# Kernel tuning notes

Measured on AMD Instinct MI355X. Metric: run time of the kernel, lower is better.

Reference implementation:

```python
import jax, jax.numpy as jnp
import numpy as np

D_MODEL = 512
NHEAD = 8
D_K = D_MODEL // NHEAD


def setup_inputs() -> dict:
    key = jax.random.key(0)
    ks = jax.random.split(key, 9)
    s = 1.0 / np.sqrt(D_MODEL)
    x = jax.random.normal(ks[0], (2, 2048, D_MODEL), dtype=jnp.float32)
    # torch Linear weights: [out_features, in_features]
    Wq = jax.random.uniform(ks[1], (D_MODEL, D_MODEL), jnp.float32, -s, s)
    bq = jax.random.uniform(ks[2], (D_MODEL,), jnp.float32, -s, s)
    Wk = jax.random.uniform(ks[3], (D_MODEL, D_MODEL), jnp.float32, -s, s)
    bk = jax.random.uniform(ks[4], (D_MODEL,), jnp.float32, -s, s)
    Wv = jax.random.uniform(ks[5], (D_MODEL, D_MODEL), jnp.float32, -s, s)
    bv = jax.random.uniform(ks[6], (D_MODEL,), jnp.float32, -s, s)
    Wo = jax.random.uniform(ks[7], (D_MODEL, D_MODEL), jnp.float32, -s, s)
    bo = jax.random.uniform(ks[8], (D_MODEL,), jnp.float32, -s, s)
    return {"x": x, "Wq": Wq, "bq": bq, "Wk": Wk, "bk": bk,
            "Wv": Wv, "bv": bv, "Wo": Wo, "bo": bo}


def reference(x, Wq, bq, Wk, bk, Wv, bv, Wo, bo):
    B, S, D = x.shape
    H, Dk = NHEAD, D_K

    def proj(W, b):
        # torch Linear: x @ W.T + b -> [B, S, D] -> [B, H, S, Dk]
        y = jnp.einsum('bsd,ed->bse', x, W) + b
        return y.reshape(B, S, H, Dk).transpose(0, 2, 1, 3)

    q = proj(Wq, bq)
    k = proj(Wk, bk)
    v = proj(Wv, bv)

    scores = jnp.einsum('bhqd,bhkd->bhqk', q, k) / jnp.sqrt(jnp.float32(Dk))
    attn = jax.nn.softmax(scores, axis=-1)  # explicit O(S^2) attention matrix
    out = jnp.einsum('bhqk,bhkd->bhqd', attn, v)
    out = out.transpose(0, 2, 1, 3).reshape(B, S, D)
    return jnp.einsum('bsd,ed->bse', out, Wo) + bo
```

## Files before the change

### kernel.cpp

```cpp
#include <hip/hip_runtime.h>

typedef __bf16 bf16_t;
typedef bf16_t bf16x8 __attribute__((ext_vector_type(8)));
typedef bf16_t bf16x4 __attribute__((ext_vector_type(4)));
typedef float  floatx4 __attribute__((ext_vector_type(4)));

#define D_MODEL 512
#define NHEAD   8
#define DK      64
#define BATCH   2
#define SEQ     2048
#define MTOT    (BATCH*SEQ)
#define QSCALE  0.18033688011112042591f

static __device__ __forceinline__ floatx4 mfma16(bf16x8 a, bf16x8 b, floatx4 c) {
    return __builtin_amdgcn_mfma_f32_16x16x32_bf16(a, b, c, 0, 0, 0);
}

__global__ __launch_bounds__(256)
void qkv_proj(const float* __restrict__ x,
              const float* __restrict__ Wq, const float* __restrict__ bq,
              const float* __restrict__ Wk, const float* __restrict__ bk,
              const float* __restrict__ Wv, const float* __restrict__ bv,
              bf16_t* __restrict__ q_ws, bf16_t* __restrict__ k_ws,
              bf16_t* __restrict__ vt_ws)
{
    __shared__ bf16_t Asq[128 * 40];
    __shared__ bf16_t Bsq[128 * 40];

    const int mtile = blockIdx.x;
    const int ntile = blockIdx.y;
    const int which = ntile >> 2;
    const int nsub  = ntile & 3;
    const float* W    = (which == 0) ? Wq : (which == 1) ? Wk : Wv;
    const float* bias = (which == 0) ? bq : (which == 1) ? bk : bv;

    const int tid  = threadIdx.x;
    const int lane = tid & 63;
    const int wave = tid >> 6;
    const int wm = wave & 1, wn = wave >> 1;
    const int l15 = lane & 15, quad = lane >> 4;

    const int m0 = mtile * 128;
    const int n0 = nsub * 128;
    const int srow = tid >> 3;
    const int sseg = tid & 7;

    floatx4 acc[4][4] = {};

    for (int k0 = 0; k0 < 512; k0 += 32) {
        __syncthreads();
        #pragma unroll
        for (int rep = 0; rep < 4; ++rep) {
            const int r = srow + rep * 32;
            const float4 va = *(const float4*)(x + (size_t)(m0 + r) * 512 + k0 + sseg * 4);
            bf16x4 pa; pa[0]=(bf16_t)va.x; pa[1]=(bf16_t)va.y; pa[2]=(bf16_t)va.z; pa[3]=(bf16_t)va.w;
            *(bf16x4*)(&Asq[r * 40 + sseg * 4]) = pa;
            const float4 vb = *(const float4*)(W + (size_t)(n0 + r) * 512 + k0 + sseg * 4);
            bf16x4 pb; pb[0]=(bf16_t)vb.x; pb[1]=(bf16_t)vb.y; pb[2]=(bf16_t)vb.z; pb[3]=(bf16_t)vb.w;
            *(bf16x4*)(&Bsq[r * 40 + sseg * 4]) = pb;
        }
        __syncthreads();

        bf16x8 af[4], bfr[4];
        #pragma unroll
        for (int i = 0; i < 4; ++i)
            af[i] = *(const bf16x8*)(&Asq[(wm * 64 + i * 16 + l15) * 40 + quad * 8]);
        #pragma unroll
        for (int j = 0; j < 4; ++j)
            bfr[j] = *(const bf16x8*)(&Bsq[(wn * 64 + j * 16 + l15) * 40 + quad * 8]);
        #pragma unroll
        for (int i = 0; i < 4; ++i)
            #pragma unroll
            for (int j = 0; j < 4; ++j)
                acc[i][j] = mfma16(af[i], bfr[j], acc[i][j]);
    }

    const float scale = (which == 0) ? QSCALE : 1.0f;
    #pragma unroll
    for (int j = 0; j < 4; ++j) {
        const int e = n0 + wn * 64 + j * 16 + l15;
        const float be = bias[e];
        const int h = e >> 6, d = e & 63;
        #pragma unroll
        for (int i = 0; i < 4; ++i) {
            const int mbase = m0 + wm * 64 + i * 16 + quad * 4;
            const int b = mbase >> 11;
            const int sl = mbase & 2047;
            floatx4 c = acc[i][j];
            if (which == 2) {
                bf16x4 pk;
                #pragma unroll
                for (int r = 0; r < 4; ++r) pk[r] = (bf16_t)(c[r] + be);
                *(bf16x4*)(vt_ws + ((size_t)((b * 8 + h) * 64 + d)) * 2048 + sl) = pk;
            } else {
                bf16_t* dst = (which == 0) ? q_ws : k_ws;
                #pragma unroll
                for (int r = 0; r < 4; ++r)
                    dst[(size_t)(b * 8 + h) * (SEQ * DK) + (size_t)(sl + r) * 64 + d] =
                        (bf16_t)((c[r] + be) * scale);
            }
        }
    }
}

#define SD 88
#define PS 68
__global__ __launch_bounds__(256, 2)
void attn_kernel(const bf16_t* __restrict__ q_ws, const bf16_t* __restrict__ k_ws,
                 const bf16_t* __restrict__ vt_ws, bf16_t* __restrict__ attn_ws)
{
    __shared__ bf16_t Ks [2][64 * SD];
    __shared__ bf16_t Vts[2][64 * SD];
    __shared__ bf16_t Ps [4][32 * PS];

    const int bh = blockIdx.x;
    const int qt = blockIdx.y;
    const int tid = threadIdx.x, lane = tid & 63, wave = tid >> 6;
    const int l15 = lane & 15, quad = lane >> 4;
    const int g  = wave >> 1;
    const int wq = wave & 1;

    const bf16_t* Qb  = q_ws  + (size_t)bh * SEQ * DK;
    const bf16_t* Kb  = k_ws  + (size_t)bh * SEQ * DK;
    const bf16_t* Vtb = vt_ws + (size_t)bh * DK * SEQ;
    bf16_t* Pw = &Ps[wave][0];

    const int srow = tid >> 3;
    const int sseg = tid & 7;

    bf16x8 aq[2][2];
    #pragma unroll
    for (int mt = 0; mt < 2; ++mt)
        #pragma unroll
        for (int c = 0; c < 2; ++c)
            aq[mt][c] = *(const bf16x8*)(Qb +
                (size_t)(qt * 64 + wq * 32 + mt * 16 + l15) * 64 + c * 32 + quad * 8);

    floatx4 O[2][4] = {};
    float rs[2][4] = {};

    for (int t = 0; t < 16; ++t) {
        __syncthreads();
        {
            const int kg0 = (2 * t + 0) * 64;
            const int kg1 = (2 * t + 1) * 64;
            #pragma unroll
            for (int rep = 0; rep < 2; ++rep) {
                const int row = srow + rep * 32;
                *(bf16x8*)(&Ks[0][row * SD + sseg * 8]) =
                    *(const bf16x8*)(Kb + (size_t)(kg0 + row) * 64 + sseg * 8);
                *(bf16x8*)(&Ks[1][row * SD + sseg * 8]) =
                    *(const bf16x8*)(Kb + (size_t)(kg1 + row) * 64 + sseg * 8);
                *(bf16x8*)(&Vts[0][row * SD + sseg * 8]) =
                    *(const bf16x8*)(Vtb + (size_t)row * 2048 + kg0 + sseg * 8);
                *(bf16x8*)(&Vts[1][row * SD + sseg * 8]) =
                    *(const bf16x8*)(Vtb + (size_t)row * 2048 + kg1 + sseg * 8);
            }
        }
        __syncthreads();

        floatx4 sc[2][4];
        #pragma unroll
        for (int kf = 0; kf < 4; ++kf) {
            bf16x8 b0 = *(const bf16x8*)(&Ks[g][(kf * 16 + l15) * SD + quad * 8]);
            bf16x8 b1 = *(const bf16x8*)(&Ks[g][(kf * 16 + l15) * SD + 32 + quad * 8]);
            #pragma unroll
            for (int mt = 0; mt < 2; ++mt) {
                floatx4 z = {0.f, 0.f, 0.f, 0.f};
                z = mfma16(aq[mt][0], b0, z);
                z = mfma16(aq[mt][1], b1, z);
                sc[mt][kf] = z;
            }
        }

        #pragma unroll
        for (int mt = 0; mt < 2; ++mt)
            #pragma unroll
            for (int kf = 0; kf < 4; ++kf)
                #pragma unroll
                for (int r = 0; r < 4; ++r) {
                    const float p = __builtin_amdgcn_exp2f(sc[mt][kf][r]);
                    rs[mt][r] += p;
                    Pw[(mt * 16 + quad * 4 + r) * PS + kf * 16 + l15] = (bf16_t)p;
                }
        asm volatile("s_waitcnt lgkmcnt(0)" ::: "memory");

        bf16x8 ap[2][2];
        #pragma unroll
        for (int mt = 0; mt < 2; ++mt) {
            bf16x4 p0 = *(const bf16x4*)(&Pw[(mt * 16 + l15) * PS + quad * 8]);
            bf16x4 p1 = *(const bf16x4*)(&Pw[(mt * 16 + l15) * PS + quad * 8 + 4]);
            bf16x4 p2 = *(const bf16x4*)(&Pw[(mt * 16 + l15) * PS + 32 + quad * 8]);
            bf16x4 p3 = *(const bf16x4*)(&Pw[(mt * 16 + l15) * PS + 32 + quad * 8 + 4]);
            ap[mt][0] = __builtin_shufflevector(p0, p1, 0, 1, 2, 3, 4, 5, 6, 7);
            ap[mt][1] = __builtin_shufflevector(p2, p3, 0, 1, 2, 3, 4, 5, 6, 7);
        }

        #pragma unroll
        for (int df = 0; df < 4; ++df) {
            bf16x8 b0 = *(const bf16x8*)(&Vts[g][(df * 16 + l15) * SD + quad * 8]);
            bf16x8 b1 = *(const bf16x8*)(&Vts[g][(df * 16 + l15) * SD + 32 + quad * 8]);
            #pragma unroll
            for (int mt = 0; mt < 2; ++mt) {
                O[mt][df] = mfma16(ap[mt][0], b0, O[mt][df]);
                O[mt][df] = mfma16(ap[mt][1], b1, O[mt][df]);
            }
        }
    }

    float* scratch = (float*)&Ks[0][0];
    __syncthreads();
    if (g == 1) {
        float* s = scratch + (size_t)(wq * 64 + lane) * 41;
        #pragma unroll
        for (int mt = 0; mt < 2; ++mt) {
            #pragma unroll
            for (int df = 0; df < 4; ++df)
                #pragma unroll
                for (int r = 0; r < 4; ++r) s[mt * 16 + df * 4 + r] = O[mt][df][r];
            #pragma unroll
            for (int r = 0; r < 4; ++r) s[32 + mt * 4 + r] = rs[mt][r];
        }
    }
    __syncthreads();
    if (g == 0) {
        const float* s = scratch + (size_t)(wq * 64 + lane) * 41;
        #pragma unroll
        for (int mt = 0; mt < 2; ++mt) {
            #pragma unroll
            for (int df = 0; df < 4; ++df)
                #pragma unroll
                for (int r = 0; r < 4; ++r) O[mt][df][r] += s[mt * 16 + df * 4 + r];
            #pragma unroll
            for (int r = 0; r < 4; ++r) rs[mt][r] += s[32 + mt * 4 + r];
        }

        #pragma unroll
        for (int off = 1; off < 16; off <<= 1)
            #pragma unroll
            for (int mt = 0; mt < 2; ++mt)
                #pragma unroll
                for (int r = 0; r < 4; ++r) rs[mt][r] += __shfl_xor(rs[mt][r], off, 64);

        const int b = bh >> 3, h = bh & 7;
        #pragma unroll
        for (int mt = 0; mt < 2; ++mt)
            #pragma unroll
            for (int r = 0; r < 4; ++r) {
                const float rinv = 1.0f / rs[mt][r];
                const int s_ = qt * 64 + wq * 32 + mt * 16 + quad * 4 + r;
                const size_t base = ((size_t)b * 2048 + s_) * 512 + h * 64;
                #pragma unroll
                for (int df = 0; df < 4; ++df)
                    attn_ws[base + df * 16 + l15] = (bf16_t)(O[mt][df][r] * rinv);
            }
    }
}

__global__ __launch_bounds__(256)
void out_proj(const bf16_t* __restrict__ attn_ws, const float* __restrict__ Wo,
              const float* __restrict__ bo, float* __restrict__ y)
{
    __shared__ bf16_t As[128 * 40];
    __shared__ bf16_t Bs[128 * 40];

    const int mtile = blockIdx.x;
    const int ntile = blockIdx.y;
    const int tid = threadIdx.x, lane = tid & 63, wave = tid >> 6;
    const int wm = wave & 1, wn = wave >> 1;
    const int l15 = lane & 15, quad = lane >> 4;
    const int m0 = mtile * 128;
    const int n0 = ntile * 128;
    const int srow = tid >> 3, sseg = tid & 7;

    floatx4 acc[4][4] = {};

    for (int k0 = 0; k0 < 512; k0 += 32) {
        __syncthreads();
        #pragma unroll
        for (int rep = 0; rep < 2; ++rep) {
            const int chunk = rep * 256 + tid;
            const int row = chunk >> 2;
            const int seg = chunk & 3;
            *(bf16x8*)(&As[row * 40 + seg * 8]) =
                *(const bf16x8*)(attn_ws + (size_t)(m0 + row) * 512 + k0 + seg * 8);
        }
        #pragma unroll
        for (int rep = 0; rep < 4; ++rep) {
            const int r = srow + rep * 32;
            const float4 vb = *(const float4*)(Wo + (size_t)(n0 + r) * 512 + k0 + sseg * 4);
            bf16x4 pb; pb[0]=(bf16_t)vb.x; pb[1]=(bf16_t)vb.y; pb[2]=(bf16_t)vb.z; pb[3]=(bf16_t)vb.w;
            *(bf16x4*)(&Bs[r * 40 + sseg * 4]) = pb;
        }
        __syncthreads();

        bf16x8 af[4], bfr[4];
        #pragma unroll
        for (int i = 0; i < 4; ++i)
            af[i] = *(const bf16x8*)(&As[(wm * 64 + i * 16 + l15) * 40 + quad * 8]);
        #pragma unroll
        for (int j = 0; j < 4; ++j)
            bfr[j] = *(const bf16x8*)(&Bs[(wn * 64 + j * 16 + l15) * 40 + quad * 8]);
        #pragma unroll
        for (int i = 0; i < 4; ++i)
            #pragma unroll
            for (int j = 0; j < 4; ++j)
                acc[i][j] = mfma16(af[i], bfr[j], acc[i][j]);
    }

    #pragma unroll
    for (int j = 0; j < 4; ++j) {
        const int e = n0 + wn * 64 + j * 16 + l15;
        const float be = bo[e];
        #pragma unroll
        for (int i = 0; i < 4; ++i) {
            const int mb = m0 + wm * 64 + i * 16 + quad * 4;
            #pragma unroll
            for (int r = 0; r < 4; ++r)
                y[(size_t)(mb + r) * 512 + e] = acc[i][j][r] + be;
        }
    }
}

extern "C" void kernel_launch(void* const* d_in, const int* in_sizes, int n_in,
                              void* d_out, int out_size, void* d_ws, size_t ws_size,
                              hipStream_t stream) {
    (void)in_sizes; (void)n_in; (void)out_size; (void)ws_size;
    const float* x  = (const float*)d_in[0];
    const float* Wq = (const float*)d_in[1];
    const float* bq = (const float*)d_in[2];
    const float* Wk = (const float*)d_in[3];
    const float* bk = (const float*)d_in[4];
    const float* Wv = (const float*)d_in[5];
    const float* bv = (const float*)d_in[6];
    const float* Wo = (const float*)d_in[7];
    const float* bo = (const float*)d_in[8];

    bf16_t* qws  = (bf16_t*)d_ws;
    bf16_t* kws  = qws  + (size_t)MTOT * D_MODEL;
    bf16_t* vtws = kws  + (size_t)MTOT * D_MODEL;
    bf16_t* aws  = vtws + (size_t)MTOT * D_MODEL;

    qkv_proj   <<<dim3(32, 12), 256, 0, stream>>>(x, Wq, bq, Wk, bk, Wv, bv, qws, kws, vtws);
    attn_kernel<<<dim3(16, 32), 256, 0, stream>>>(qws, kws, vtws, aws);
    out_proj   <<<dim3(32, 4),  256, 0, stream>>>(aws, Wo, bo, (float*)d_out);
}
```

Before: 151.8 us.

## Pre-convert inputs to bf16 and stage tiles via direct global-to-LDS loads

Adds a conversion kernel that casts x and all four weight matrices to bf16 once, so the projection GEMMs read bf16 instead of converting fp32 in every tile load. All three compute kernels now fill shared memory with global_load_lds (direct global-to-LDS DMA) using unpadded 32-wide rows. The attention kernel raises its occupancy hint to 3 blocks per CU, and the output projection halves its M tile to launch twice as many blocks. The cost is an extra launch plus a round trip of x through the workspace, and unpadded LDS rows may cause more bank conflicts on fragment reads.

```diff
diff --git a/kernel.cpp b/kernel.cpp
--- a/kernel.cpp
+++ b/kernel.cpp
@@ -17,58 +17,84 @@
     return __builtin_amdgcn_mfma_f32_16x16x32_bf16(a, b, c, 0, 0, 0);
 }
 
+static __device__ __forceinline__ void glds16(bf16_t* lds, const bf16_t* g) {
+    __builtin_amdgcn_global_load_lds(
+        (const __attribute__((address_space(1))) unsigned int*)g,
+        (__attribute__((address_space(3))) unsigned int*)lds,
+        16, 0, 0);
+}
+
 __global__ __launch_bounds__(256)
-void qkv_proj(const float* __restrict__ x,
-              const float* __restrict__ Wq, const float* __restrict__ bq,
-              const float* __restrict__ Wk, const float* __restrict__ bk,
-              const float* __restrict__ Wv, const float* __restrict__ bv,
+void to_bf16(const float* __restrict__ x,
+             const float* __restrict__ Wq, const float* __restrict__ Wk,
+             const float* __restrict__ Wv, const float* __restrict__ Wo,
+             bf16_t* __restrict__ xb, bf16_t* __restrict__ wqb,
+             bf16_t* __restrict__ wkb, bf16_t* __restrict__ wvb,
+             bf16_t* __restrict__ wob)
+{
+    const int blk = blockIdx.x;
+    const float* src; bf16_t* dst; size_t base;
+    if      (blk < 1024) { src = x;  dst = xb;  base = (size_t)blk * 2048; }
+    else if (blk < 1152) { src = Wq; dst = wqb; base = (size_t)(blk - 1024) * 2048; }
+    else if (blk < 1280) { src = Wk; dst = wkb; base = (size_t)(blk - 1152) * 2048; }
+    else if (blk < 1408) { src = Wv; dst = wvb; base = (size_t)(blk - 1280) * 2048; }
+    else                 { src = Wo; dst = wob; base = (size_t)(blk - 1408) * 2048; }
+    const size_t off = base + (size_t)threadIdx.x * 8;
+    const float4 a = *(const float4*)(src + off);
+    const float4 b = *(const float4*)(src + off + 4);
+    bf16x8 p;
+    p[0]=(bf16_t)a.x; p[1]=(bf16_t)a.y; p[2]=(bf16_t)a.z; p[3]=(bf16_t)a.w;
+    p[4]=(bf16_t)b.x; p[5]=(bf16_t)b.y; p[6]=(bf16_t)b.z; p[7]=(bf16_t)b.w;
+    *(bf16x8*)(dst + off) = p;
+}
+
+__global__ __launch_bounds__(256)
+void qkv_proj(const bf16_t* __restrict__ xb,
+              const bf16_t* __restrict__ wqb, const float* __restrict__ bq,
+              const bf16_t* __restrict__ wkb, const float* __restrict__ bk,
+              const bf16_t* __restrict__ wvb, const float* __restrict__ bv,
               bf16_t* __restrict__ q_ws, bf16_t* __restrict__ k_ws,
               bf16_t* __restrict__ vt_ws)
 {
-    __shared__ bf16_t Asq[128 * 40];
-    __shared__ bf16_t Bsq[128 * 40];
+    __shared__ bf16_t As[128 * 32];
+    __shared__ bf16_t Bs[128 * 32];
 
     const int mtile = blockIdx.x;
     const int ntile = blockIdx.y;
     const int which = ntile >> 2;
     const int nsub  = ntile & 3;
-    const float* W    = (which == 0) ? Wq : (which == 1) ? Wk : Wv;
-    const float* bias = (which == 0) ? bq : (which == 1) ? bk : bv;
+    const bf16_t* W   = (which == 0) ? wqb : (which == 1) ? wkb : wvb;
+    const float* bias = (which == 0) ? bq  : (which == 1) ? bk  : bv;
 
     const int tid  = threadIdx.x;
     const int lane = tid & 63;
     const int wave = tid >> 6;
     const int wm = wave & 1, wn = wave >> 1;
     const int l15 = lane & 15, quad = lane >> 4;
-
     const int m0 = mtile * 128;
     const int n0 = nsub * 128;
-    const int srow = tid >> 3;
-    const int sseg = tid & 7;
+    const int lr = lane >> 2;
+    const int lc = (lane & 3) * 8;
 
     floatx4 acc[4][4] = {};
 
     for (int k0 = 0; k0 < 512; k0 += 32) {
         __syncthreads();
         #pragma unroll
-        for (int rep = 0; rep < 4; ++rep) {
-            const int r = srow + rep * 32;
-            const float4 va = *(const float4*)(x + (size_t)(m0 + r) * 512 + k0 + sseg * 4);
-            bf16x4 pa; pa[0]=(bf16_t)va.x; pa[1]=(bf16_t)va.y; pa[2]=(bf16_t)va.z; pa[3]=(bf16_t)va.w;
-            *(bf16x4*)(&Asq[r * 40 + sseg * 4]) = pa;
-            const float4 vb = *(const float4*)(W + (size_t)(n0 + r) * 512 + k0 + sseg * 4);
-            bf16x4 pb; pb[0]=(bf16_t)vb.x; pb[1]=(bf16_t)vb.y; pb[2]=(bf16_t)vb.z; pb[3]=(bf16_t)vb.w;
-            *(bf16x4*)(&Bsq[r * 40 + sseg * 4]) = pb;
+        for (int q = 0; q < 2; ++q) {
+            const int r = wave * 32 + q * 16;
+            glds16(&As[r * 32], xb + (size_t)(m0 + r + lr) * 512 + k0 + lc);
+            glds16(&Bs[r * 32], W  + (size_t)(n0 + r + lr) * 512 + k0 + lc);
         }
         __syncthreads();
 
         bf16x8 af[4], bfr[4];
         #pragma unroll
         for (int i = 0; i < 4; ++i)
-            af[i] = *(const bf16x8*)(&Asq[(wm * 64 + i * 16 + l15) * 40 + quad * 8]);
+            af[i] = *(const bf16x8*)(&As[(wm * 64 + i * 16 + l15) * 32 + quad * 8]);
         #pragma unroll
         for (int j = 0; j < 4; ++j)
-            bfr[j] = *(const bf16x8*)(&Bsq[(wn * 64 + j * 16 + l15) * 40 + quad * 8]);
+            bfr[j] = *(const bf16x8*)(&Bs[(wn * 64 + j * 16 + l15) * 32 + quad * 8]);
         #pragma unroll
         for (int i = 0; i < 4; ++i)
             #pragma unroll
@@ -104,14 +130,12 @@
     }
 }
 
-#define SD 88
 #define PS 68
-__global__ __launch_bounds__(256, 2)
+__global__ __launch_bounds__(256, 3)
 void attn_kernel(const bf16_t* __restrict__ q_ws, const bf16_t* __restrict__ k_ws,
                  const bf16_t* __restrict__ vt_ws, bf16_t* __restrict__ attn_ws)
 {
-    __shared__ bf16_t Ks [2][64 * SD];
-    __shared__ bf16_t Vts[2][64 * SD];
+    __shared__ bf16_t KV[2][2][2][64 * 32];
     __shared__ bf16_t Ps [4][32 * PS];
 
     const int bh = blockIdx.x;
@@ -120,15 +144,13 @@
     const int l15 = lane & 15, quad = lane >> 4;
     const int g  = wave >> 1;
     const int wq = wave & 1;
+    const int lr = lane >> 2, lc = (lane & 3) * 8;
 
     const bf16_t* Qb  = q_ws  + (size_t)bh * SEQ * DK;
     const bf16_t* Kb  = k_ws  + (size_t)bh * SEQ * DK;
     const bf16_t* Vtb = vt_ws + (size_t)bh * DK * SEQ;
     bf16_t* Pw = &Ps[wave][0];
 
-    const int srow = tid >> 3;
-    const int sseg = tid & 7;
-
     bf16x8 aq[2][2];
     #pragma unroll
     for (int mt = 0; mt < 2; ++mt)
@@ -143,28 +165,24 @@
     for (int t = 0; t < 16; ++t) {
         __syncthreads();
         {
-            const int kg0 = (2 * t + 0) * 64;
-            const int kg1 = (2 * t + 1) * 64;
-            #pragma unroll
-            for (int rep = 0; rep < 2; ++rep) {
-                const int row = srow + rep * 32;
-                *(bf16x8*)(&Ks[0][row * SD + sseg * 8]) =
-                    *(const bf16x8*)(Kb + (size_t)(kg0 + row) * 64 + sseg * 8);
-                *(bf16x8*)(&Ks[1][row * SD + sseg * 8]) =
-                    *(const bf16x8*)(Kb + (size_t)(kg1 + row) * 64 + sseg * 8);
-                *(bf16x8*)(&Vts[0][row * SD + sseg * 8]) =
-                    *(const bf16x8*)(Vtb + (size_t)row * 2048 + kg0 + sseg * 8);
-                *(bf16x8*)(&Vts[1][row * SD + sseg * 8]) =
-                    *(const bf16x8*)(Vtb + (size_t)row * 2048 + kg1 + sseg * 8);
-            }
+            const int r0 = wave * 16;
+            const int kg0 = t * 128, kg1 = t * 128 + 64;
+            glds16(&KV[0][0][0][r0 * 32], Kb + (size_t)(kg0 + r0 + lr) * 64 + lc);
+            glds16(&KV[0][0][1][r0 * 32], Kb + (size_t)(kg0 + r0 + lr) * 64 + 32 + lc);
+            glds16(&KV[0][1][0][r0 * 32], Kb + (size_t)(kg1 + r0 + lr) * 64 + lc);
+            glds16(&KV[0][1][1][r0 * 32], Kb + (size_t)(kg1 + r0 + lr) * 64 + 32 + lc);
+            glds16(&KV[1][0][0][r0 * 32], Vtb + (size_t)(r0 + lr) * 2048 + kg0 + lc);
+            glds16(&KV[1][0][1][r0 * 32], Vtb + (size_t)(r0 + lr) * 2048 + kg0 + 32 + lc);
+            glds16(&KV[1][1][0][r0 * 32], Vtb + (size_t)(r0 + lr) * 2048 + kg1 + lc);
+            glds16(&KV[1][1][1][r0 * 32], Vtb + (size_t)(r0 + lr) * 2048 + kg1 + 32 + lc);
         }
         __syncthreads();
 
         floatx4 sc[2][4];
         #pragma unroll
         for (int kf = 0; kf < 4; ++kf) {
-            bf16x8 b0 = *(const bf16x8*)(&Ks[g][(kf * 16 + l15) * SD + quad * 8]);
-            bf16x8 b1 = *(const bf16x8*)(&Ks[g][(kf * 16 + l15) * SD + 32 + quad * 8]);
+            bf16x8 b0 = *(const bf16x8*)(&KV[0][g][0][(kf * 16 + l15) * 32 + quad * 8]);
+            bf16x8 b1 = *(const bf16x8*)(&KV[0][g][1][(kf * 16 + l15) * 32 + quad * 8]);
             #pragma unroll
             for (int mt = 0; mt < 2; ++mt) {
                 floatx4 z = {0.f, 0.f, 0.f, 0.f};
@@ -199,8 +217,8 @@
 
         #pragma unroll
         for (int df = 0; df < 4; ++df) {
-            bf16x8 b0 = *(const bf16x8*)(&Vts[g][(df * 16 + l15) * SD + quad * 8]);
-            bf16x8 b1 = *(const bf16x8*)(&Vts[g][(df * 16 + l15) * SD + 32 + quad * 8]);
+            bf16x8 b0 = *(const bf16x8*)(&KV[1][g][0][(df * 16 + l15) * 32 + quad * 8]);
+            bf16x8 b1 = *(const bf16x8*)(&KV[1][g][1][(df * 16 + l15) * 32 + quad * 8]);
             #pragma unroll
             for (int mt = 0; mt < 2; ++mt) {
                 O[mt][df] = mfma16(ap[mt][0], b0, O[mt][df]);
@@ -209,7 +227,7 @@
         }
     }
 
-    float* scratch = (float*)&Ks[0][0];
+    float* scratch = (float*)&KV[0][0][0][0];
     __syncthreads();
     if (g == 1) {
         float* s = scratch + (size_t)(wq * 64 + lane) * 41;
@@ -259,51 +277,42 @@
 }
 
 __global__ __launch_bounds__(256)
-void out_proj(const bf16_t* __restrict__ attn_ws, const float* __restrict__ Wo,
+void out_proj(const bf16_t* __restrict__ attn_ws, const bf16_t* __restrict__ wob,
               const float* __restrict__ bo, float* __restrict__ y)
 {
-    __shared__ bf16_t As[128 * 40];
-    __shared__ bf16_t Bs[128 * 40];
+    __shared__ bf16_t As[64 * 32];
+    __shared__ bf16_t Bs[128 * 32];
 
     const int mtile = blockIdx.x;
     const int ntile = blockIdx.y;
     const int tid = threadIdx.x, lane = tid & 63, wave = tid >> 6;
     const int wm = wave & 1, wn = wave >> 1;
     const int l15 = lane & 15, quad = lane >> 4;
-    const int m0 = mtile * 128;
+    const int m0 = mtile * 64;
     const int n0 = ntile * 128;
-    const int srow = tid >> 3, sseg = tid & 7;
-
-    floatx4 acc[4][4] = {};
+    const int lr = lane >> 2, lc = (lane & 3) * 8;
+
+    floatx4 acc[2][4] = {};
 
     for (int k0 = 0; k0 < 512; k0 += 32) {
         __syncthreads();
-        #pragma unroll
-        for (int rep = 0; rep < 2; ++rep) {
-            const int chunk = rep * 256 + tid;
-            const int row = chunk >> 2;
-            const int seg = chunk & 3;
-            *(bf16x8*)(&As[row * 40 + seg * 8]) =
-                *(const bf16x8*)(attn_ws + (size_t)(m0 + row) * 512 + k0 + seg * 8);
-        }
-        #pragma unroll
-        for (int rep = 0; rep < 4; ++rep) {
-            const int r = srow + rep * 32;
-            const float4 vb = *(const float4*)(Wo + (size_t)(n0 + r) * 512 + k0 + sseg * 4);
-            bf16x4 pb; pb[0]=(bf16_t)vb.x; pb[1]=(bf16_t)vb.y; pb[2]=(bf16_t)vb.z; pb[3]=(bf16_t)vb.w;
-            *(bf16x4*)(&Bs[r * 40 + sseg * 4]) = pb;
-        }
-        __syncthreads();
-
-        bf16x8 af[4], bfr[4];
-        #pragma unroll
-        for (int i = 0; i < 4; ++i)
-            af[i] = *(const bf16x8*)(&As[(wm * 64 + i * 16 + l15) * 40 + quad * 8]);
+        glds16(&As[wave * 16 * 32], attn_ws + (size_t)(m0 + wave * 16 + lr) * 512 + k0 + lc);
+        #pragma unroll
+        for (int q = 0; q < 2; ++q) {
+            const int r = wave * 32 + q * 16;
+            glds16(&Bs[r * 32], wob + (size_t)(n0 + r + lr) * 512 + k0 + lc);
+        }
+        __syncthreads();
+
+        bf16x8 af[2], bfr[4];
+        #pragma unroll
+        for (int i = 0; i < 2; ++i)
+            af[i] = *(const bf16x8*)(&As[(wm * 32 + i * 16 + l15) * 32 + quad * 8]);
         #pragma unroll
         for (int j = 0; j < 4; ++j)
-            bfr[j] = *(const bf16x8*)(&Bs[(wn * 64 + j * 16 + l15) * 40 + quad * 8]);
-        #pragma unroll
-        for (int i = 0; i < 4; ++i)
+            bfr[j] = *(const bf16x8*)(&Bs[(wn * 64 + j * 16 + l15) * 32 + quad * 8]);
+        #pragma unroll
+        for (int i = 0; i < 2; ++i)
             #pragma unroll
             for (int j = 0; j < 4; ++j)
                 acc[i][j] = mfma16(af[i], bfr[j], acc[i][j]);
@@ -314,8 +323,8 @@
         const int e = n0 + wn * 64 + j * 16 + l15;
         const float be = bo[e];
         #pragma unroll
-        for (int i = 0; i < 4; ++i) {
-            const int mb = m0 + wm * 64 + i * 16 + quad * 4;
+        for (int i = 0; i < 2; ++i) {
+            const int mb = m0 + wm * 32 + i * 16 + quad * 4;
             #pragma unroll
             for (int r = 0; r < 4; ++r)
                 y[(size_t)(mb + r) * 512 + e] = acc[i][j][r] + be;
@@ -337,12 +346,18 @@
     const float* Wo = (const float*)d_in[7];
     const float* bo = (const float*)d_in[8];
 
-    bf16_t* qws  = (bf16_t*)d_ws;
+    bf16_t* xb   = (bf16_t*)d_ws;
+    bf16_t* wqb  = xb   + (size_t)MTOT * D_MODEL;
+    bf16_t* wkb  = wqb  + (size_t)D_MODEL * D_MODEL;
+    bf16_t* wvb  = wkb  + (size_t)D_MODEL * D_MODEL;
+    bf16_t* wob  = wvb  + (size_t)D_MODEL * D_MODEL;
+    bf16_t* qws  = wob  + (size_t)D_MODEL * D_MODEL;
     bf16_t* kws  = qws  + (size_t)MTOT * D_MODEL;
     bf16_t* vtws = kws  + (size_t)MTOT * D_MODEL;
     bf16_t* aws  = vtws + (size_t)MTOT * D_MODEL;
 
-    qkv_proj   <<<dim3(32, 12), 256, 0, stream>>>(x, Wq, bq, Wk, bk, Wv, bv, qws, kws, vtws);
+    to_bf16    <<<1536, 256, 0, stream>>>(x, Wq, Wk, Wv, Wo, xb, wqb, wkb, wvb, wob);
+    qkv_proj   <<<dim3(32, 12), 256, 0, stream>>>(xb, wqb, bq, wkb, bk, wvb, bv, qws, kws, vtws);
     attn_kernel<<<dim3(16, 32), 256, 0, stream>>>(qws, kws, vtws, aws);
-    out_proj   <<<dim3(32, 4),  256, 0, stream>>>(aws, Wo, bo, (float*)d_out);
-}
+    out_proj   <<<dim3(64, 4),  256, 0, stream>>>(aws, wob, bo, (float*)d_out);
+}
```

Result: faster. 137.6 us (-9.3%).
